# Kernel optimization log

Measured on AMD Instinct MI355X. Metric: run time of the kernel, lower is better.

The kernel has to match this reference:

```python
import jax, jax.numpy as jnp
import numpy as np

IN_DIM, HID_DIM, OUT_DIM, HEADS = 128, 256, 128, 4
N0, N1, N2 = 80000, 40000, 8000
E1, E2 = 400000, 128000
NEG_SLOPE = 0.2


def _glorot(key, shape):
    fan = shape[0] + shape[-1]
    lim = jnp.sqrt(6.0 / fan)
    return jax.random.uniform(key, shape, jnp.float32, -lim, lim)


def setup_inputs() -> dict:
    key = jax.random.key(0)
    ks = jax.random.split(key, 16)
    inp = {
        "x": jax.random.normal(ks[0], (N0, IN_DIM), jnp.float32),
        "edge_src1": jax.random.randint(ks[1], (E1,), 0, N0),
        "edge_dst1": jax.random.randint(ks[2], (E1,), 0, N1),
        "edge_src2": jax.random.randint(ks[3], (E2,), 0, N1),
        "edge_dst2": jax.random.randint(ks[4], (E2,), 0, N2),
        # GAT1: in_dim -> heads*in_dim (shared lin for src/dst in PyG when in_channels is int)
        "W1": _glorot(ks[5], (IN_DIM, HEADS * IN_DIM)),
        "att_src1": _glorot(ks[6], (HEADS, IN_DIM)),
        "att_dst1": _glorot(ks[7], (HEADS, IN_DIM)),
        "b1": jnp.zeros((HEADS * IN_DIM,), jnp.float32),
        # GAT2: hid_dim -> hid_dim, heads=1
        "W2": _glorot(ks[8], (HID_DIM, HID_DIM)),
        "att_src2": _glorot(ks[9], (1, HID_DIM)),
        "att_dst2": _glorot(ks[10], (1, HID_DIM)),
        "b2": jnp.zeros((HID_DIM,), jnp.float32),
        # Conv1d kernel_size=1 == per-node linear
        "conv1_w": _glorot(ks[11], (HID_DIM, HEADS * IN_DIM)),
        "conv1_b": jnp.zeros((HID_DIM,), jnp.float32),
        "conv2_w": _glorot(ks[12], (OUT_DIM, HID_DIM)),
        "conv2_b": jnp.zeros((OUT_DIM,), jnp.float32),
    }
    return inp


def _gat(x_src, x_dst, src, dst, W, att_s, att_d, bias, n_dst, heads, out_c):
    h_src = (x_src @ W).reshape(-1, heads, out_c)   # [Ns,H,C]
    h_dst = (x_dst @ W).reshape(-1, heads, out_c)   # [Nd,H,C]
    a_s = jnp.einsum('nhc,hc->nh', h_src, att_s)    # [Ns,H]
    a_d = jnp.einsum('nhc,hc->nh', h_dst, att_d)    # [Nd,H]
    alpha = jax.nn.leaky_relu(a_s[src] + a_d[dst], NEG_SLOPE)  # [E,H]
    m = jax.ops.segment_max(alpha, dst, num_segments=n_dst)
    alpha = jnp.exp(alpha - jnp.maximum(m, -1e30)[dst])
    denom = jax.ops.segment_sum(alpha, dst, num_segments=n_dst)
    alpha = alpha / (denom[dst] + 1e-16)
    msg = h_src[src] * alpha[:, :, None]            # [E,H,C]
    out = jax.ops.segment_sum(msg, dst, num_segments=n_dst)
    return out.reshape(n_dst, heads * out_c) + bias


def reference(x, edge_src1, edge_dst1, edge_src2, edge_dst2,
              W1, att_src1, att_dst1, b1, W2, att_src2, att_dst2, b2,
              conv1_w, conv1_b, conv2_w, conv2_b):
    # layer 0: GAT1 (heads=4, concat) + Conv1d(512->256, k=1)
    h = _gat(x, x[:N1], edge_src1, edge_dst1, W1, att_src1, att_dst1, b1,
             N1, HEADS, IN_DIM)                      # [N1, 512]
    h = h @ conv1_w.T + conv1_b                      # [N1, 256]
    # layer 1: GAT2 (heads=1) + Conv1d(256->128, k=1)
    h = _gat(h, h[:N2], edge_src2, edge_dst2, W2, att_src2, att_dst2, b2,
             N2, 1, HID_DIM)                         # [N2, 256]
    h = h @ conv2_w.T + conv2_b                      # [N2, 128]
    return h
```

## Files before the change

### kernel.cpp

```cpp
#include <hip/hip_runtime.h>
#include <math.h>

#define IN_DIM 128
#define HID_DIM 256
#define OUT_DIM 128
#define HEADS 4
#define N0 80000
#define N1 40000
#define N2 8000
#define E1 400000
#define E2 128000
#define NEG 0.2f
#define NB1 40
#define NB2 8

typedef __attribute__((ext_vector_type(8))) short bf16x8;
typedef __attribute__((ext_vector_type(4))) float f32x4;

__device__ __forceinline__ float bf2f(short s) {
  return __uint_as_float(((unsigned int)(unsigned short)s) << 16);
}
__device__ __forceinline__ short f2bf(float f) {
  unsigned int u = __float_as_uint(f);
  unsigned int r = (u + 0x7FFFu + ((u >> 16) & 1u)) >> 16;
  return (short)r;
}
__device__ __forceinline__ float lrelu(float t) {
  return t > 0.f ? t : NEG * t;
}

__global__ __launch_bounds__(256) void prep_all_kernel(
    const float* __restrict__ W1, const float* __restrict__ att_s1,
    const float* __restrict__ att_d1, const float* __restrict__ b1,
    const float* __restrict__ c1w, const float* __restrict__ c1b,
    const float* __restrict__ W2, const float* __restrict__ att_s2,
    const float* __restrict__ att_d2, const float* __restrict__ b2,
    const float* __restrict__ c2w, const float* __restrict__ c2b,
    short* __restrict__ M1t, float* __restrict__ p1,
    float* __restrict__ bias1p, short* __restrict__ M2t,
    float* __restrict__ p2, float* __restrict__ bias2p) {
  int b = blockIdx.x, t = threadIdx.x;
  if (b < 512) {
    int g = b * 256 + t;
    int o = g >> 9, kf = g & 511;
    int h = kf >> 7, k = kf & 127;
    float acc = 0.f;
    for (int c = 0; c < 128; c++)
      acc += W1[(long)k * 512 + h * 128 + c] * c1w[(long)o * 512 + h * 128 + c];
    M1t[g] = f2bf(acc);
  } else if (b < 640) {
    int g = (b - 512) * 256 + t;
    int o = g >> 8, k = g & 255;
    float acc = 0.f;
    for (int c = 0; c < 256; c++)
      acc += W2[(long)k * 256 + c] * c2w[(long)o * 256 + c];
    M2t[g] = f2bf(acc);
  } else if (b < 644) {
    int g = (b - 640) * 256 + t;
    int i = g >> 3, hh = g & 7;
    int h = hh & 3;
    const float* att = (hh < 4) ? att_s1 : att_d1;
    float acc = 0.f;
    for (int c = 0; c < 128; c++)
      acc += W1[(long)i * 512 + h * 128 + c] * att[h * 128 + c];
    p1[g] = acc;
  } else if (b == 644) {
    if (t < 256) {
      float acc = c1b[t];
      for (int c = 0; c < 512; c++) acc += b1[c] * c1w[(long)t * 512 + c];
      bias1p[t] = acc;
    }
  } else if (b < 647) {
    int g = (b - 645) * 256 + t;
    if (g < 512) {
      int k = g >> 1, j = g & 1;
      const float* att = j ? att_d2 : att_s2;
      float acc = 0.f;
      for (int c = 0; c < 256; c++) acc += W2[(long)k * 256 + c] * att[c];
      p2[g] = acc;
    }
  } else {
    if (t < 128) {
      float acc = c2b[t];
      for (int c = 0; c < 256; c++) acc += b2[c] * c2w[(long)t * 256 + c];
      bias2p[t] = acc;
    }
  }
}

template<bool BIAS, bool OUTBF>
__global__ __launch_bounds__(256) void mm_bf16_kernel(
    const short* __restrict__ A, const short* __restrict__ Bt,
    const float* __restrict__ bias, void* __restrict__ Cv,
    int M, int N, int K) {
  __shared__ short As[128][40];
  __shared__ short Bs[64][40];
  int tid = threadIdx.x;
  int bn = blockIdx.x * 64;
  int bm = blockIdx.y * 128;
  int w = tid >> 6;
  int lane = tid & 63;
  int lr = lane & 15, kb = lane >> 4;
  f32x4 acc[2][4] = {};

  for (int k0 = 0; k0 < K; k0 += 32) {
#pragma unroll
    for (int i = 0; i < 2; i++) {
      int seg = tid + i * 256;
      int row = seg >> 2, part = seg & 3;
      int gm = bm + row;
      bf16x8 v = {0, 0, 0, 0, 0, 0, 0, 0};
      if (gm < M) v = *(const bf16x8*)(A + (long)gm * K + k0 + part * 8);
      *(bf16x8*)&As[row][part * 8] = v;
    }
    {
      int r = tid >> 2, part = tid & 3;
      *(bf16x8*)&Bs[r][part * 8] =
          *(const bf16x8*)(Bt + (long)(bn + r) * K + k0 + part * 8);
    }
    __syncthreads();
    bf16x8 a0 = *(const bf16x8*)&As[w * 32 + lr][kb * 8];
    bf16x8 a1 = *(const bf16x8*)&As[w * 32 + 16 + lr][kb * 8];
    bf16x8 b0 = *(const bf16x8*)&Bs[lr][kb * 8];
    bf16x8 b1 = *(const bf16x8*)&Bs[16 + lr][kb * 8];
    bf16x8 b2 = *(const bf16x8*)&Bs[32 + lr][kb * 8];
    bf16x8 b3 = *(const bf16x8*)&Bs[48 + lr][kb * 8];
    acc[0][0] = __builtin_amdgcn_mfma_f32_16x16x32_bf16(a0, b0, acc[0][0], 0, 0, 0);
    acc[0][1] = __builtin_amdgcn_mfma_f32_16x16x32_bf16(a0, b1, acc[0][1], 0, 0, 0);
    acc[0][2] = __builtin_amdgcn_mfma_f32_16x16x32_bf16(a0, b2, acc[0][2], 0, 0, 0);
    acc[0][3] = __builtin_amdgcn_mfma_f32_16x16x32_bf16(a0, b3, acc[0][3], 0, 0, 0);
    acc[1][0] = __builtin_amdgcn_mfma_f32_16x16x32_bf16(a1, b0, acc[1][0], 0, 0, 0);
    acc[1][1] = __builtin_amdgcn_mfma_f32_16x16x32_bf16(a1, b1, acc[1][1], 0, 0, 0);
    acc[1][2] = __builtin_amdgcn_mfma_f32_16x16x32_bf16(a1, b2, acc[1][2], 0, 0, 0);
    acc[1][3] = __builtin_amdgcn_mfma_f32_16x16x32_bf16(a1, b3, acc[1][3], 0, 0, 0);
    __syncthreads();
  }
#pragma unroll
  for (int mt = 0; mt < 2; mt++) {
#pragma unroll
    for (int nt = 0; nt < 4; nt++) {
#pragma unroll
      for (int r = 0; r < 4; r++) {
        int row = bm + w * 32 + mt * 16 + kb * 4 + r;
        if (row >= M) continue;
        int col = bn + nt * 16 + lr;
        float v = acc[mt][nt][r];
        if (BIAS) v += bias[col];
        if (OUTBF)
          ((short*)Cv)[(long)row * N + col] = f2bf(v);
        else
          ((float*)Cv)[(long)row * N + col] = v;
      }
    }
  }
}

__global__ __launch_bounds__(256) void cast_attn1_kernel(
    const float* __restrict__ x, const float* __restrict__ p1,
    short* __restrict__ x_bf, float* __restrict__ a_s,
    float* __restrict__ a_d) {
  int tid = threadIdx.x;
  int l16 = tid & 15;
  long nb = ((long)blockIdx.x * 16 + (tid >> 4)) * 4;
  int ch0 = l16 * 8;
  float xs[4][8];
#pragma unroll
  for (int i = 0; i < 4; i++) {
    float4 a = *(const float4*)&x[(nb + i) * 128 + ch0];
    float4 b = *(const float4*)&x[(nb + i) * 128 + ch0 + 4];
    xs[i][0] = a.x; xs[i][1] = a.y; xs[i][2] = a.z; xs[i][3] = a.w;
    xs[i][4] = b.x; xs[i][5] = b.y; xs[i][6] = b.z; xs[i][7] = b.w;
  }
#pragma unroll
  for (int i = 0; i < 4; i++) {
    short4 o1, o2;
    o1.x = f2bf(xs[i][0]); o1.y = f2bf(xs[i][1]);
    o1.z = f2bf(xs[i][2]); o1.w = f2bf(xs[i][3]);
    o2.x = f2bf(xs[i][4]); o2.y = f2bf(xs[i][5]);
    o2.z = f2bf(xs[i][6]); o2.w = f2bf(xs[i][7]);
    *(short4*)&x_bf[(nb + i) * 128 + ch0] = o1;
    *(short4*)&x_bf[(nb + i) * 128 + ch0 + 4] = o2;
  }
  float acc[4][8] = {};
#pragma unroll
  for (int c = 0; c < 8; c++) {
    float4 pA = *(const float4*)&p1[(ch0 + c) * 8];
    float4 pB = *(const float4*)&p1[(ch0 + c) * 8 + 4];
#pragma unroll
    for (int i = 0; i < 4; i++) {
      float xc = xs[i][c];
      acc[i][0] += xc * pA.x; acc[i][1] += xc * pA.y;
      acc[i][2] += xc * pA.z; acc[i][3] += xc * pA.w;
      acc[i][4] += xc * pB.x; acc[i][5] += xc * pB.y;
      acc[i][6] += xc * pB.z; acc[i][7] += xc * pB.w;
    }
  }
#pragma unroll
  for (int off = 1; off <= 8; off <<= 1) {
#pragma unroll
    for (int i = 0; i < 4; i++)
#pragma unroll
      for (int k = 0; k < 8; k++) acc[i][k] += __shfl_xor(acc[i][k], off);
  }
  if (l16 == 0) {
#pragma unroll
    for (int i = 0; i < 4; i++) {
      long n = nb + i;
      *(float4*)&a_s[n * 4] =
          make_float4(acc[i][0], acc[i][1], acc[i][2], acc[i][3]);
      if (n < N1)
        *(float4*)&a_d[n * 4] =
            make_float4(acc[i][4], acc[i][5], acc[i][6], acc[i][7]);
    }
  }
}

__global__ __launch_bounds__(256) void attn2_kernel(
    const short* __restrict__ hid1, const float* __restrict__ p2,
    float* __restrict__ a_s, float* __restrict__ a_d) {
  int tid = threadIdx.x;
  int l32 = tid & 31;
  long n = (long)blockIdx.x * 8 + (tid >> 5);
  if (n >= N1) return;
  int ch0 = l32 * 8;
  bf16x8 hv = *(const bf16x8*)&hid1[n * 256 + ch0];
  float s = 0.f, d = 0.f;
#pragma unroll
  for (int c = 0; c < 8; c += 2) {
    float4 q = *(const float4*)&p2[(ch0 + c) * 2];
    float h0 = bf2f(hv[c]), h1 = bf2f(hv[c + 1]);
    s += h0 * q.x + h1 * q.z;
    d += h0 * q.y + h1 * q.w;
  }
#pragma unroll
  for (int off = 1; off <= 16; off <<= 1) {
    s += __shfl_xor(s, off);
    d += __shfl_xor(d, off);
  }
  if (l32 == 0) {
    a_s[n] = s;
    if (n < N2) a_d[n] = d;
  }
}

__global__ void hist12_kernel(const int* __restrict__ ed1,
                              const int* __restrict__ ed2,
                              int* __restrict__ deg1, int* __restrict__ deg2,
                              int* __restrict__ rank1,
                              int* __restrict__ rank2) {
  int e = blockIdx.x * blockDim.x + threadIdx.x;
  if (e < E1) {
    rank1[e] = atomicAdd(&deg1[ed1[e]], 1);
  } else {
    int e2 = e - E1;
    if (e2 < E2) rank2[e2] = atomicAdd(&deg2[ed2[e2]], 1);
  }
}

__global__ __launch_bounds__(256) void scanA12_kernel(
    const int* __restrict__ deg1, const int* __restrict__ deg2,
    int* __restrict__ part) {
  __shared__ int red[256];
  int b = blockIdx.x;
  const int* deg;
  int n, base;
  if (b < NB1) { deg = deg1; n = N1; base = b * 1024; }
  else { deg = deg2; n = N2; base = (b - NB1) * 1024; }
  int s = 0;
  for (int i = threadIdx.x; i < 1024; i += 256) {
    int idx = base + i;
    if (idx < n) s += deg[idx];
  }
  red[threadIdx.x] = s;
  __syncthreads();
  for (int off = 128; off >= 1; off >>= 1) {
    if (threadIdx.x < off) red[threadIdx.x] += red[threadIdx.x + off];
    __syncthreads();
  }
  if (threadIdx.x == 0) part[b] = red[0];
}

__global__ __launch_bounds__(256) void scanC12_kernel(
    const int* __restrict__ deg1, const int* __restrict__ deg2,
    const int* __restrict__ part, int* __restrict__ offs1,
    int* __restrict__ offs2) {
  __shared__ int tsum[256];
  int b = blockIdx.x;
  const int* deg;
  int n, pbase, bl;
  int* offs;
  if (b < NB1) { deg = deg1; n = N1; offs = offs1; pbase = 0; bl = b; }
  else { deg = deg2; n = N2; offs = offs2; pbase = NB1; bl = b - NB1; }
  int boff = 0;
  for (int i = 0; i < bl; i++) boff += part[pbase + i];
  int base = bl * 1024;
  int v[4];
  int s = 0;
#pragma unroll
  for (int k = 0; k < 4; k++) {
    int idx = base + threadIdx.x * 4 + k;
    v[k] = (idx < n) ? deg[idx] : 0;
    s += v[k];
  }
  tsum[threadIdx.x] = s;
  __syncthreads();
  for (int off = 1; off < 256; off <<= 1) {
    int t = (threadIdx.x >= off) ? tsum[threadIdx.x - off] : 0;
    __syncthreads();
    tsum[threadIdx.x] += t;
    __syncthreads();
  }
  int run = boff + ((threadIdx.x > 0) ? tsum[threadIdx.x - 1] : 0);
#pragma unroll
  for (int k = 0; k < 4; k++) {
    int idx = base + threadIdx.x * 4 + k;
    if (idx < n) {
      offs[idx] = run;
      run += v[k];
    }
  }
  if (bl == 0 && threadIdx.x == 0) offs[n] = (b < NB1) ? E1 : E2;
}

__global__ void scatter1_kernel(const int* __restrict__ src,
                                const int* __restrict__ dst, int E,
                                const int* __restrict__ offs,
                                const int* __restrict__ rank,
                                const float* __restrict__ a_s,
                                const float* __restrict__ a_d,
                                int* __restrict__ csr_src,
                                float* __restrict__ csr_w) {
  int e = blockIdx.x * blockDim.x + threadIdx.x;
  if (e >= E) return;
  int s = src[e], d = dst[e];
  int p = offs[d] + rank[e];
  csr_src[p] = s;
  float4 as = *(const float4*)&a_s[s * 4];
  float4 ad = *(const float4*)&a_d[d * 4];
  float4 t;
  t.x = __expf(lrelu(as.x + ad.x));
  t.y = __expf(lrelu(as.y + ad.y));
  t.z = __expf(lrelu(as.z + ad.z));
  t.w = __expf(lrelu(as.w + ad.w));
  *(float4*)&csr_w[(long)p * 4] = t;
}

__global__ void scatter2_kernel(const int* __restrict__ src,
                                const int* __restrict__ dst, int E,
                                const int* __restrict__ offs,
                                const int* __restrict__ rank,
                                const float* __restrict__ a_s,
                                const float* __restrict__ a_d,
                                int* __restrict__ csr_src,
                                float* __restrict__ csr_w) {
  int e = blockIdx.x * blockDim.x + threadIdx.x;
  if (e >= E) return;
  int s = src[e], d = dst[e];
  int p = offs[d] + rank[e];
  csr_src[p] = s;
  csr_w[p] = __expf(lrelu(a_s[s] + a_d[d]));
}

__global__ __launch_bounds__(256) void gather1_kernel(
    const short* __restrict__ x, const int* __restrict__ csr_src,
    const float* __restrict__ csr_w, const int* __restrict__ offs,
    short* __restrict__ z1) {
  int wid = threadIdx.x >> 6, lane = threadIdx.x & 63;
  long d = (long)blockIdx.x * 4 + wid;
  if (d >= N1) return;
  int lo = offs[d], deg = offs[d + 1] - lo;
  int half = lane >> 5, l32 = lane & 31;
  float acc[4][4] = {};
  float den[4] = {};
#pragma unroll 2
  for (int j = half; j < deg; j += 2) {
    long p = lo + j;
    int s = csr_src[p];
    float4 w = *(const float4*)&csr_w[p * 4];
    short4 xv = *(const short4*)&x[(long)s * 128 + l32 * 4];
    float f0 = bf2f(xv.x), f1 = bf2f(xv.y), f2 = bf2f(xv.z), f3 = bf2f(xv.w);
    den[0] += w.x; den[1] += w.y; den[2] += w.z; den[3] += w.w;
    acc[0][0] += w.x * f0; acc[0][1] += w.x * f1; acc[0][2] += w.x * f2; acc[0][3] += w.x * f3;
    acc[1][0] += w.y * f0; acc[1][1] += w.y * f1; acc[1][2] += w.y * f2; acc[1][3] += w.y * f3;
    acc[2][0] += w.z * f0; acc[2][1] += w.z * f1; acc[2][2] += w.z * f2; acc[2][3] += w.z * f3;
    acc[3][0] += w.w * f0; acc[3][1] += w.w * f1; acc[3][2] += w.w * f2; acc[3][3] += w.w * f3;
  }
#pragma unroll
  for (int h = 0; h < 4; h++) {
    den[h] += __shfl_xor(den[h], 32);
#pragma unroll
    for (int k = 0; k < 4; k++) acc[h][k] += __shfl_xor(acc[h][k], 32);
  }
  if (half == 0) {
#pragma unroll
    for (int h = 0; h < 4; h++) {
      float inv = 1.f / (den[h] + 1e-16f);
      short4 o;
      o.x = f2bf(acc[h][0] * inv);
      o.y = f2bf(acc[h][1] * inv);
      o.z = f2bf(acc[h][2] * inv);
      o.w = f2bf(acc[h][3] * inv);
      *(short4*)&z1[d * 512 + h * 128 + l32 * 4] = o;
    }
  }
}

__global__ __launch_bounds__(256) void gather2_kernel(
    const short* __restrict__ hid1, const int* __restrict__ csr_src,
    const float* __restrict__ csr_w, const int* __restrict__ offs,
    short* __restrict__ z2) {
  int wid = threadIdx.x >> 6, lane = threadIdx.x & 63;
  long d = (long)blockIdx.x * 4 + wid;
  if (d >= N2) return;
  int lo = offs[d], deg = offs[d + 1] - lo;
  int half = lane >> 5, l32 = lane & 31;
  int ch0 = l32 * 8;
  float acc[8] = {};
  float den = 0.f;
#pragma unroll 2
  for (int j = half; j < deg; j += 2) {
    long p = lo + j;
    int s = csr_src[p];
    float w = csr_w[p];
    den += w;
    bf16x8 v = *(const bf16x8*)&hid1[(long)s * 256 + ch0];
#pragma unroll
    for (int k = 0; k < 8; k++) acc[k] += w * bf2f(v[k]);
  }
  den += __shfl_xor(den, 32);
#pragma unroll
  for (int k = 0; k < 8; k++) acc[k] += __shfl_xor(acc[k], 32);
  if (half == 0) {
    float inv = 1.f / (den + 1e-16f);
    bf16x8 o;
#pragma unroll
    for (int k = 0; k < 8; k++) o[k] = f2bf(acc[k] * inv);
    *(bf16x8*)&z2[d * 256 + ch0] = o;
  }
}

extern "C" void kernel_launch(void* const* d_in, const int* in_sizes, int n_in,
                              void* d_out, int out_size, void* d_ws,
                              size_t ws_size, hipStream_t stream) {
  const float* x = (const float*)d_in[0];
  const int* es1 = (const int*)d_in[1];
  const int* ed1 = (const int*)d_in[2];
  const int* es2 = (const int*)d_in[3];
  const int* ed2 = (const int*)d_in[4];
  const float* W1 = (const float*)d_in[5];
  const float* att_s1 = (const float*)d_in[6];
  const float* att_d1 = (const float*)d_in[7];
  const float* b1 = (const float*)d_in[8];
  const float* W2 = (const float*)d_in[9];
  const float* att_s2 = (const float*)d_in[10];
  const float* att_d2 = (const float*)d_in[11];
  const float* b2 = (const float*)d_in[12];
  const float* c1w = (const float*)d_in[13];
  const float* c1b = (const float*)d_in[14];
  const float* c2w = (const float*)d_in[15];
  const float* c2b = (const float*)d_in[16];
  float* out = (float*)d_out;

  char* ws = (char*)d_ws;
  size_t off = 0;
  auto alloc = [&](size_t bytes) {
    void* p = ws + off;
    off += (bytes + 255) & ~(size_t)255;
    return p;
  };
  short* x_bf = (short*)alloc((size_t)N0 * 128 * 2);
  short* z1 = (short*)alloc((size_t)N1 * 512 * 2);
  short* hid1 = (short*)alloc((size_t)N1 * 256 * 2);
  short* z2 = (short*)alloc((size_t)N2 * 256 * 2);
  float* p1 = (float*)alloc(128 * 8 * 4);
  short* M1t = (short*)alloc(256 * 512 * 2);
  float* bias1p = (float*)alloc(256 * 4);
  float* p2 = (float*)alloc(256 * 2 * 4);
  short* M2t = (short*)alloc(128 * 256 * 2);
  float* bias2p = (float*)alloc(128 * 4);
  float* as1 = (float*)alloc((size_t)N0 * 4 * 4);
  float* ad1v = (float*)alloc((size_t)N1 * 4 * 4);
  float* as2 = (float*)alloc((size_t)N1 * 4);
  float* ad2v = (float*)alloc((size_t)N2 * 4);
  int* deg1 = (int*)alloc((size_t)N1 * 4);
  int* deg2 = (int*)alloc((size_t)N2 * 4);
  int* offs1 = (int*)alloc((size_t)(N1 + 1) * 4);
  int* rank1 = (int*)alloc((size_t)E1 * 4);
  int* offs2 = (int*)alloc((size_t)(N2 + 1) * 4);
  int* rank2 = (int*)alloc((size_t)E2 * 4);
  int* part12 = (int*)alloc(64 * 4);
  int* csr_src1 = (int*)alloc((size_t)E1 * 4);
  float* csr_w1 = (float*)alloc((size_t)E1 * 4 * 4);
  int* csr_src2 = (int*)alloc((size_t)E2 * 4);
  float* csr_w2 = (float*)alloc((size_t)E2 * 4);

  hipMemsetAsync(deg1, 0, (size_t)N1 * 4 + (size_t)N2 * 4, stream);

  prep_all_kernel<<<648, 256, 0, stream>>>(W1, att_s1, att_d1, b1, c1w, c1b,
                                           W2, att_s2, att_d2, b2, c2w, c2b,
                                           M1t, p1, bias1p, M2t, p2, bias2p);
  cast_attn1_kernel<<<N0 / 64, 256, 0, stream>>>(x, p1, x_bf, as1, ad1v);
  hist12_kernel<<<(E1 + E2 + 255) / 256, 256, 0, stream>>>(ed1, ed2, deg1,
                                                           deg2, rank1, rank2);
  scanA12_kernel<<<NB1 + NB2, 256, 0, stream>>>(deg1, deg2, part12);
  scanC12_kernel<<<NB1 + NB2, 256, 0, stream>>>(deg1, deg2, part12, offs1,
                                                offs2);
  scatter1_kernel<<<(E1 + 255) / 256, 256, 0, stream>>>(
      es1, ed1, E1, offs1, rank1, as1, ad1v, csr_src1, csr_w1);
  gather1_kernel<<<(N1 + 3) / 4, 256, 0, stream>>>(x_bf, csr_src1, csr_w1,
                                                   offs1, z1);
  mm_bf16_kernel<true, true><<<dim3(4, (N1 + 127) / 128), 256, 0, stream>>>(
      z1, M1t, bias1p, hid1, N1, 256, 512);

  attn2_kernel<<<(N1 + 7) / 8, 256, 0, stream>>>(hid1, p2, as2, ad2v);
  scatter2_kernel<<<(E2 + 255) / 256, 256, 0, stream>>>(
      es2, ed2, E2, offs2, rank2, as2, ad2v, csr_src2, csr_w2);
  gather2_kernel<<<(N2 + 3) / 4, 256, 0, stream>>>(hid1, csr_src2, csr_w2,
                                                   offs2, z2);
  mm_bf16_kernel<true, false><<<dim3(2, (N2 + 127) / 128), 256, 0, stream>>>(
      z2, M2t, bias2p, out, N2, 128, 256);
}
```

Before: 200.0 us.

## Merge prep, cast and histogram kernels into phased launches; widen GEMM K-tile

Replaces the memset plus the three separate prep, cast/attention and histogram launches with two kernels. Phase 0 zeroes the degree arrays and computes p1. Phase 1 runs the weight folding, the x cast with attention logits, and the edge histogram as independent block ranges of one grid. This cuts launch overhead and lets independent work overlap. Separately, the bf16 MFMA GEMM K-tile goes from 32 to 64, halving the number of shared-memory sync iterations at the cost of more LDS per block.

```diff
diff --git a/kernel.cpp b/kernel.cpp
--- a/kernel.cpp
+++ b/kernel.cpp
@@ -13,6 +13,12 @@
 #define NEG 0.2f
 #define NB1 40
 #define NB2 8
+#define ZERO_BLKS 47
+#define PH0_BLKS (ZERO_BLKS + 4)
+#define PREP_BLKS 644
+#define CAST_BLKS 1250
+#define HIST_BLKS 2063
+#define PH1_BLKS (PREP_BLKS + CAST_BLKS + HIST_BLKS)
 
 typedef __attribute__((ext_vector_type(8))) short bf16x8;
 typedef __attribute__((ext_vector_type(4))) float f32x4;
@@ -29,34 +35,16 @@
   return t > 0.f ? t : NEG * t;
 }
 
-__global__ __launch_bounds__(256) void prep_all_kernel(
-    const float* __restrict__ W1, const float* __restrict__ att_s1,
-    const float* __restrict__ att_d1, const float* __restrict__ b1,
-    const float* __restrict__ c1w, const float* __restrict__ c1b,
-    const float* __restrict__ W2, const float* __restrict__ att_s2,
-    const float* __restrict__ att_d2, const float* __restrict__ b2,
-    const float* __restrict__ c2w, const float* __restrict__ c2b,
-    short* __restrict__ M1t, float* __restrict__ p1,
-    float* __restrict__ bias1p, short* __restrict__ M2t,
-    float* __restrict__ p2, float* __restrict__ bias2p) {
+__global__ __launch_bounds__(256) void phase0_kernel(
+    float4* __restrict__ zp, const float* __restrict__ W1,
+    const float* __restrict__ att_s1, const float* __restrict__ att_d1,
+    float* __restrict__ p1) {
   int b = blockIdx.x, t = threadIdx.x;
-  if (b < 512) {
-    int g = b * 256 + t;
-    int o = g >> 9, kf = g & 511;
-    int h = kf >> 7, k = kf & 127;
-    float acc = 0.f;
-    for (int c = 0; c < 128; c++)
-      acc += W1[(long)k * 512 + h * 128 + c] * c1w[(long)o * 512 + h * 128 + c];
-    M1t[g] = f2bf(acc);
-  } else if (b < 640) {
-    int g = (b - 512) * 256 + t;
-    int o = g >> 8, k = g & 255;
-    float acc = 0.f;
-    for (int c = 0; c < 256; c++)
-      acc += W2[(long)k * 256 + c] * c2w[(long)o * 256 + c];
-    M2t[g] = f2bf(acc);
-  } else if (b < 644) {
-    int g = (b - 640) * 256 + t;
+  if (b < ZERO_BLKS) {
+    int i = b * 256 + t;
+    if (i < 12000) zp[i] = make_float4(0.f, 0.f, 0.f, 0.f);
+  } else {
+    int g = (b - ZERO_BLKS) * 256 + t;
     int i = g >> 3, hh = g & 7;
     int h = hh & 3;
     const float* att = (hh < 4) ? att_s1 : att_d1;
@@ -64,26 +52,125 @@
     for (int c = 0; c < 128; c++)
       acc += W1[(long)i * 512 + h * 128 + c] * att[h * 128 + c];
     p1[g] = acc;
-  } else if (b == 644) {
-    if (t < 256) {
-      float acc = c1b[t];
-      for (int c = 0; c < 512; c++) acc += b1[c] * c1w[(long)t * 512 + c];
-      bias1p[t] = acc;
-    }
-  } else if (b < 647) {
-    int g = (b - 645) * 256 + t;
-    if (g < 512) {
-      int k = g >> 1, j = g & 1;
-      const float* att = j ? att_d2 : att_s2;
+  }
+}
+
+__global__ __launch_bounds__(256) void phase1_kernel(
+    const float* __restrict__ W1, const float* __restrict__ b1,
+    const float* __restrict__ c1w, const float* __restrict__ c1b,
+    const float* __restrict__ W2, const float* __restrict__ att_s2,
+    const float* __restrict__ att_d2, const float* __restrict__ b2,
+    const float* __restrict__ c2w, const float* __restrict__ c2b,
+    short* __restrict__ M1t, const float* __restrict__ p1,
+    float* __restrict__ bias1p, short* __restrict__ M2t,
+    float* __restrict__ p2, float* __restrict__ bias2p,
+    const float* __restrict__ x, short* __restrict__ x_bf,
+    float* __restrict__ a_s, float* __restrict__ a_d,
+    const int* __restrict__ ed1, const int* __restrict__ ed2,
+    int* __restrict__ deg1, int* __restrict__ deg2, int* __restrict__ rank1,
+    int* __restrict__ rank2) {
+  int b = blockIdx.x, t = threadIdx.x;
+  if (b < PREP_BLKS) {
+    if (b < 512) {
+      int g = b * 256 + t;
+      int o = g >> 9, kf = g & 511;
+      int h = kf >> 7, k = kf & 127;
       float acc = 0.f;
-      for (int c = 0; c < 256; c++) acc += W2[(long)k * 256 + c] * att[c];
-      p2[g] = acc;
+      for (int c = 0; c < 128; c++)
+        acc +=
+            W1[(long)k * 512 + h * 128 + c] * c1w[(long)o * 512 + h * 128 + c];
+      M1t[g] = f2bf(acc);
+    } else if (b < 640) {
+      int g = (b - 512) * 256 + t;
+      int o = g >> 8, k = g & 255;
+      float acc = 0.f;
+      for (int c = 0; c < 256; c++)
+        acc += W2[(long)k * 256 + c] * c2w[(long)o * 256 + c];
+      M2t[g] = f2bf(acc);
+    } else if (b == 640) {
+      if (t < 256) {
+        float acc = c1b[t];
+        for (int c = 0; c < 512; c++) acc += b1[c] * c1w[(long)t * 512 + c];
+        bias1p[t] = acc;
+      }
+    } else if (b < 643) {
+      int g = (b - 641) * 256 + t;
+      if (g < 512) {
+        int k = g >> 1, j = g & 1;
+        const float* att = j ? att_d2 : att_s2;
+        float acc = 0.f;
+        for (int c = 0; c < 256; c++) acc += W2[(long)k * 256 + c] * att[c];
+        p2[g] = acc;
+      }
+    } else {
+      if (t < 128) {
+        float acc = c2b[t];
+        for (int c = 0; c < 256; c++) acc += b2[c] * c2w[(long)t * 256 + c];
+        bias2p[t] = acc;
+      }
+    }
+  } else if (b < PREP_BLKS + CAST_BLKS) {
+    int bb = b - PREP_BLKS;
+    int l16 = t & 15;
+    long nb = ((long)bb * 16 + (t >> 4)) * 4;
+    int ch0 = l16 * 8;
+    float xs[4][8];
+#pragma unroll
+    for (int i = 0; i < 4; i++) {
+      float4 a = *(const float4*)&x[(nb + i) * 128 + ch0];
+      float4 bv = *(const float4*)&x[(nb + i) * 128 + ch0 + 4];
+      xs[i][0] = a.x; xs[i][1] = a.y; xs[i][2] = a.z; xs[i][3] = a.w;
+      xs[i][4] = bv.x; xs[i][5] = bv.y; xs[i][6] = bv.z; xs[i][7] = bv.w;
+    }
+#pragma unroll
+    for (int i = 0; i < 4; i++) {
+      short4 o1, o2;
+      o1.x = f2bf(xs[i][0]); o1.y = f2bf(xs[i][1]);
+      o1.z = f2bf(xs[i][2]); o1.w = f2bf(xs[i][3]);
+      o2.x = f2bf(xs[i][4]); o2.y = f2bf(xs[i][5]);
+      o2.z = f2bf(xs[i][6]); o2.w = f2bf(xs[i][7]);
+      *(short4*)&x_bf[(nb + i) * 128 + ch0] = o1;
+      *(short4*)&x_bf[(nb + i) * 128 + ch0 + 4] = o2;
+    }
+    float acc[4][8] = {};
+#pragma unroll
+    for (int c = 0; c < 8; c++) {
+      float4 pA = *(const float4*)&p1[(ch0 + c) * 8];
+      float4 pB = *(const float4*)&p1[(ch0 + c) * 8 + 4];
+#pragma unroll
+      for (int i = 0; i < 4; i++) {
+        float xc = xs[i][c];
+        acc[i][0] += xc * pA.x; acc[i][1] += xc * pA.y;
+        acc[i][2] += xc * pA.z; acc[i][3] += xc * pA.w;
+        acc[i][4] += xc * pB.x; acc[i][5] += xc * pB.y;
+        acc[i][6] += xc * pB.z; acc[i][7] += xc * pB.w;
+      }
+    }
+#pragma unroll
+    for (int off = 1; off <= 8; off <<= 1) {
+#pragma unroll
+      for (int i = 0; i < 4; i++)
+#pragma unroll
+        for (int k = 0; k < 8; k++) acc[i][k] += __shfl_xor(acc[i][k], off);
+    }
+    if (l16 == 0) {
+#pragma unroll
+      for (int i = 0; i < 4; i++) {
+        long n = nb + i;
+        *(float4*)&a_s[n * 4] =
+            make_float4(acc[i][0], acc[i][1], acc[i][2], acc[i][3]);
+        if (n < N1)
+          *(float4*)&a_d[n * 4] =
+              make_float4(acc[i][4], acc[i][5], acc[i][6], acc[i][7]);
+      }
     }
   } else {
-    if (t < 128) {
-      float acc = c2b[t];
-      for (int c = 0; c < 256; c++) acc += b2[c] * c2w[(long)t * 256 + c];
-      bias2p[t] = acc;
+    int e = (b - PREP_BLKS - CAST_BLKS) * 256 + t;
+    if (e < E1) {
+      rank1[e] = atomicAdd(&deg1[ed1[e]], 1);
+    } else {
+      int e2 = e - E1;
+      if (e2 < E2) rank2[e2] = atomicAdd(&deg2[ed2[e2]], 1);
     }
   }
 }
@@ -93,8 +180,8 @@
     const short* __restrict__ A, const short* __restrict__ Bt,
     const float* __restrict__ bias, void* __restrict__ Cv,
     int M, int N, int K) {
-  __shared__ short As[128][40];
-  __shared__ short Bs[64][40];
+  __shared__ short As[128][72];
+  __shared__ short Bs[64][72];
   int tid = threadIdx.x;
   int bn = blockIdx.x * 64;
   int bm = blockIdx.y * 128;
@@ -103,36 +190,41 @@
   int lr = lane & 15, kb = lane >> 4;
   f32x4 acc[2][4] = {};
 
-  for (int k0 = 0; k0 < K; k0 += 32) {
-#pragma unroll
-    for (int i = 0; i < 2; i++) {
+  for (int k0 = 0; k0 < K; k0 += 64) {
+#pragma unroll
+    for (int i = 0; i < 4; i++) {
       int seg = tid + i * 256;
-      int row = seg >> 2, part = seg & 3;
+      int row = seg >> 3, part = seg & 7;
       int gm = bm + row;
       bf16x8 v = {0, 0, 0, 0, 0, 0, 0, 0};
       if (gm < M) v = *(const bf16x8*)(A + (long)gm * K + k0 + part * 8);
       *(bf16x8*)&As[row][part * 8] = v;
     }
-    {
-      int r = tid >> 2, part = tid & 3;
+#pragma unroll
+    for (int i = 0; i < 2; i++) {
+      int seg = tid + i * 256;
+      int r = seg >> 3, part = seg & 7;
       *(bf16x8*)&Bs[r][part * 8] =
           *(const bf16x8*)(Bt + (long)(bn + r) * K + k0 + part * 8);
     }
     __syncthreads();
-    bf16x8 a0 = *(const bf16x8*)&As[w * 32 + lr][kb * 8];
-    bf16x8 a1 = *(const bf16x8*)&As[w * 32 + 16 + lr][kb * 8];
-    bf16x8 b0 = *(const bf16x8*)&Bs[lr][kb * 8];
-    bf16x8 b1 = *(const bf16x8*)&Bs[16 + lr][kb * 8];
-    bf16x8 b2 = *(const bf16x8*)&Bs[32 + lr][kb * 8];
-    bf16x8 b3 = *(const bf16x8*)&Bs[48 + lr][kb * 8];
-    acc[0][0] = __builtin_amdgcn_mfma_f32_16x16x32_bf16(a0, b0, acc[0][0], 0, 0, 0);
-    acc[0][1] = __builtin_amdgcn_mfma_f32_16x16x32_bf16(a0, b1, acc[0][1], 0, 0, 0);
-    acc[0][2] = __builtin_amdgcn_mfma_f32_16x16x32_bf16(a0, b2, acc[0][2], 0, 0, 0);
-    acc[0][3] = __builtin_amdgcn_mfma_f32_16x16x32_bf16(a0, b3, acc[0][3], 0, 0, 0);
-    acc[1][0] = __builtin_amdgcn_mfma_f32_16x16x32_bf16(a1, b0, acc[1][0], 0, 0, 0);
-    acc[1][1] = __builtin_amdgcn_mfma_f32_16x16x32_bf16(a1, b1, acc[1][1], 0, 0, 0);
-    acc[1][2] = __builtin_amdgcn_mfma_f32_16x16x32_bf16(a1, b2, acc[1][2], 0, 0, 0);
-    acc[1][3] = __builtin_amdgcn_mfma_f32_16x16x32_bf16(a1, b3, acc[1][3], 0, 0, 0);
+#pragma unroll
+    for (int kk = 0; kk < 64; kk += 32) {
+      bf16x8 a0 = *(const bf16x8*)&As[w * 32 + lr][kk + kb * 8];
+      bf16x8 a1 = *(const bf16x8*)&As[w * 32 + 16 + lr][kk + kb * 8];
+      bf16x8 b0 = *(const bf16x8*)&Bs[lr][kk + kb * 8];
+      bf16x8 b1 = *(const bf16x8*)&Bs[16 + lr][kk + kb * 8];
+      bf16x8 b2 = *(const bf16x8*)&Bs[32 + lr][kk + kb * 8];
+      bf16x8 b3 = *(const bf16x8*)&Bs[48 + lr][kk + kb * 8];
+      acc[0][0] = __builtin_amdgcn_mfma_f32_16x16x32_bf16(a0, b0, acc[0][0], 0, 0, 0);
+      acc[0][1] = __builtin_amdgcn_mfma_f32_16x16x32_bf16(a0, b1, acc[0][1], 0, 0, 0);
+      acc[0][2] = __builtin_amdgcn_mfma_f32_16x16x32_bf16(a0, b2, acc[0][2], 0, 0, 0);
+      acc[0][3] = __builtin_amdgcn_mfma_f32_16x16x32_bf16(a0, b3, acc[0][3], 0, 0, 0);
+      acc[1][0] = __builtin_amdgcn_mfma_f32_16x16x32_bf16(a1, b0, acc[1][0], 0, 0, 0);
+      acc[1][1] = __builtin_amdgcn_mfma_f32_16x16x32_bf16(a1, b1, acc[1][1], 0, 0, 0);
+      acc[1][2] = __builtin_amdgcn_mfma_f32_16x16x32_bf16(a1, b2, acc[1][2], 0, 0, 0);
+      acc[1][3] = __builtin_amdgcn_mfma_f32_16x16x32_bf16(a1, b3, acc[1][3], 0, 0, 0);
+    }
     __syncthreads();
   }
 #pragma unroll
@@ -155,66 +247,6 @@
   }
 }
 
-__global__ __launch_bounds__(256) void cast_attn1_kernel(
-    const float* __restrict__ x, const float* __restrict__ p1,
-    short* __restrict__ x_bf, float* __restrict__ a_s,
-    float* __restrict__ a_d) {
-  int tid = threadIdx.x;
-  int l16 = tid & 15;
-  long nb = ((long)blockIdx.x * 16 + (tid >> 4)) * 4;
-  int ch0 = l16 * 8;
-  float xs[4][8];
-#pragma unroll
-  for (int i = 0; i < 4; i++) {
-    float4 a = *(const float4*)&x[(nb + i) * 128 + ch0];
-    float4 b = *(const float4*)&x[(nb + i) * 128 + ch0 + 4];
-    xs[i][0] = a.x; xs[i][1] = a.y; xs[i][2] = a.z; xs[i][3] = a.w;
-    xs[i][4] = b.x; xs[i][5] = b.y; xs[i][6] = b.z; xs[i][7] = b.w;
-  }
-#pragma unroll
-  for (int i = 0; i < 4; i++) {
-    short4 o1, o2;
-    o1.x = f2bf(xs[i][0]); o1.y = f2bf(xs[i][1]);
-    o1.z = f2bf(xs[i][2]); o1.w = f2bf(xs[i][3]);
-    o2.x = f2bf(xs[i][4]); o2.y = f2bf(xs[i][5]);
-    o2.z = f2bf(xs[i][6]); o2.w = f2bf(xs[i][7]);
-    *(short4*)&x_bf[(nb + i) * 128 + ch0] = o1;
-    *(short4*)&x_bf[(nb + i) * 128 + ch0 + 4] = o2;
-  }
-  float acc[4][8] = {};
-#pragma unroll
-  for (int c = 0; c < 8; c++) {
-    float4 pA = *(const float4*)&p1[(ch0 + c) * 8];
-    float4 pB = *(const float4*)&p1[(ch0 + c) * 8 + 4];
-#pragma unroll
-    for (int i = 0; i < 4; i++) {
-      float xc = xs[i][c];
-      acc[i][0] += xc * pA.x; acc[i][1] += xc * pA.y;
-      acc[i][2] += xc * pA.z; acc[i][3] += xc * pA.w;
-      acc[i][4] += xc * pB.x; acc[i][5] += xc * pB.y;
-      acc[i][6] += xc * pB.z; acc[i][7] += xc * pB.w;
-    }
-  }
-#pragma unroll
-  for (int off = 1; off <= 8; off <<= 1) {
-#pragma unroll
-    for (int i = 0; i < 4; i++)
-#pragma unroll
-      for (int k = 0; k < 8; k++) acc[i][k] += __shfl_xor(acc[i][k], off);
-  }
-  if (l16 == 0) {
-#pragma unroll
-    for (int i = 0; i < 4; i++) {
-      long n = nb + i;
-      *(float4*)&a_s[n * 4] =
-          make_float4(acc[i][0], acc[i][1], acc[i][2], acc[i][3]);
-      if (n < N1)
-        *(float4*)&a_d[n * 4] =
-            make_float4(acc[i][4], acc[i][5], acc[i][6], acc[i][7]);
-    }
-  }
-}
-
 __global__ __launch_bounds__(256) void attn2_kernel(
     const short* __restrict__ hid1, const float* __restrict__ p2,
     float* __restrict__ a_s, float* __restrict__ a_d) {
@@ -240,20 +272,6 @@
   if (l32 == 0) {
     a_s[n] = s;
     if (n < N2) a_d[n] = d;
-  }
-}
-
-__global__ void hist12_kernel(const int* __restrict__ ed1,
-                              const int* __restrict__ ed2,
-                              int* __restrict__ deg1, int* __restrict__ deg2,
-                              int* __restrict__ rank1,
-                              int* __restrict__ rank2) {
-  int e = blockIdx.x * blockDim.x + threadIdx.x;
-  if (e < E1) {
-    rank1[e] = atomicAdd(&deg1[ed1[e]], 1);
-  } else {
-    int e2 = e - E1;
-    if (e2 < E2) rank2[e2] = atomicAdd(&deg2[ed2[e2]], 1);
   }
 }
 
@@ -494,14 +512,13 @@
   int* csr_src2 = (int*)alloc((size_t)E2 * 4);
   float* csr_w2 = (float*)alloc((size_t)E2 * 4);
 
-  hipMemsetAsync(deg1, 0, (size_t)N1 * 4 + (size_t)N2 * 4, stream);
-
-  prep_all_kernel<<<648, 256, 0, stream>>>(W1, att_s1, att_d1, b1, c1w, c1b,
-                                           W2, att_s2, att_d2, b2, c2w, c2b,
-                                           M1t, p1, bias1p, M2t, p2, bias2p);
-  cast_attn1_kernel<<<N0 / 64, 256, 0, stream>>>(x, p1, x_bf, as1, ad1v);
-  hist12_kernel<<<(E1 + E2 + 255) / 256, 256, 0, stream>>>(ed1, ed2, deg1,
-                                                           deg2, rank1, rank2);
+  phase0_kernel<<<PH0_BLKS, 256, 0, stream>>>((float4*)deg1, W1, att_s1,
+                                              att_d1, p1);
+
+  phase1_kernel<<<PH1_BLKS, 256, 0, stream>>>(
+      W1, b1, c1w, c1b, W2, att_s2, att_d2, b2, c2w, c2b, M1t, p1, bias1p,
+      M2t, p2, bias2p, x, x_bf, as1, ad1v, ed1, ed2, deg1, deg2, rank1, rank2);
+
   scanA12_kernel<<<NB1 + NB2, 256, 0, stream>>>(deg1, deg2, part12);
   scanC12_kernel<<<NB1 + NB2, 256, 0, stream>>>(deg1, deg2, part12, offs1,
                                                 offs2);
```

Result: faster. 189.8 us (-5.1%).
